# Performance work log

Measured on AMD Instinct MI355X. Metric: run time of the kernel, lower is better.

## Reference

```python
import jax, jax.numpy as jnp
import numpy as np

H = 32          # hidden_dim (forced by targetLayer = Linear(4*32, 1))
IN = 1          # input_size per step
T = 129         # seq_len
S = 4           # 4 parallel LSTM streams: [main, f1, f2, f3]


def setup_inputs() -> dict:
    key = jax.random.key(0)
    ks = jax.random.split(key, 16)
    sc = 1.0 / np.sqrt(H)
    u = lambda k, shape: jax.random.uniform(k, shape, jnp.float32, -sc, sc)
    inp = {
        "x": jax.random.normal(ks[0], (S, T, IN), jnp.float32),
        # layer 0 (input -> hidden), stacked over the 4 LSTMs; gate order i,f,g,o
        "Wih0": u(ks[1], (S, 4 * H, IN)),
        "Whh0": u(ks[2], (S, 4 * H, H)),
        "bih0": u(ks[3], (S, 4 * H)),
        "bhh0": u(ks[4], (S, 4 * H)),
        # layer 1 (hidden -> hidden)
        "Wih1": u(ks[5], (S, 4 * H, H)),
        "Whh1": u(ks[6], (S, 4 * H, H)),
        "bih1": u(ks[7], (S, 4 * H)),
        "bhh1": u(ks[8], (S, 4 * H)),
        # output heads
        "Wt": u(ks[9], (1, 4 * H)),
        "bt": u(ks[10], (1,)),
        "Wf1": u(ks[11], (1, H)),
        "bf1": u(ks[12], (1,)),
        "Wf2": u(ks[13], (1, H)),
        "bf2": u(ks[14], (1,)),
    }
    return inp


def _cell(xin, h, c, Wih, Whh, bih, bhh):
    # xin: [S, in], h/c: [S, H]; fused 4-stream LSTM cell, PyTorch gate order i,f,g,o
    g = jnp.einsum('sgi,si->sg', Wih, xin) + jnp.einsum('sgh,sh->sg', Whh, h) + bih + bhh
    i, f, gg, o = jnp.split(g, 4, axis=-1)
    c2 = jax.nn.sigmoid(f) * c + jax.nn.sigmoid(i) * jnp.tanh(gg)
    h2 = jax.nn.sigmoid(o) * jnp.tanh(c2)
    return h2, c2


def reference(x, Wih0, Whh0, bih0, bhh0, Wih1, Whh1, bih1, bhh1, Wt, bt, Wf1, bf1, Wf2, bf2):
    z = jnp.zeros((S, H), x.dtype)

    def step(carry, xt):
        h0, c0, h1, c1 = carry
        h0, c0 = _cell(xt, h0, c0, Wih0, Whh0, bih0, bhh0)
        h1, c1 = _cell(h0, h1, c1, Wih1, Whh1, bih1, bhh1)
        return (h0, c0, h1, c1), None

    xs = jnp.transpose(x, (1, 0, 2))  # [T, S, IN]
    (h0, c0, h1, c1), _ = jax.lax.scan(step, (z, z, z, z), xs)
    hlast = h1  # [S, H], last-step top-layer output; order: main, f1, f2, f3

    targetIn = hlast.reshape(1, S * H)          # torch.cat(...).view(-1, 4H)
    targetOut = targetIn @ Wt.T + bt            # [1, 1]
    f1Out = (hlast[1:2] @ Wf1.T + bf1).reshape(1, 1, 1)
    f2Out = (hlast[2:3] @ Wf2.T + bf2).reshape(1, 1, 1)
    f3Out = (hlast[3:4] @ Wf2.T + bf2).reshape(1, 1, 1)  # original bug: reuses featureLayer2
    return (targetOut, f1Out, f2Out, f3Out)
```

## Files before the change

### kernel.cpp

```cpp
#include <hip/hip_runtime.h>


#define HDIM 32
#define SEQT 129
#define NS 4

typedef float f32x2 __attribute__((ext_vector_type(2)));

__device__ __forceinline__ float fsig(float x) {
  return __builtin_amdgcn_rcpf(1.0f + __expf(-x));
}
__device__ __forceinline__ float swap_hi(float v) {
  auto r = __builtin_amdgcn_permlane32_swap(__float_as_int(v), __float_as_int(v),
                                            false, false);
  return __int_as_float(r[1]);
}

__device__ __forceinline__ float pkdot(const f32x2* __restrict__ w,
                                       const f32x2* __restrict__ h, float seed) {
  f32x2 a0 = {seed, 0.f}, a1 = {0.f, 0.f}, a2 = {0.f, 0.f}, a3 = {0.f, 0.f};
  #pragma unroll
  for (int j = 0; j < 4; ++j) {
    a0 = __builtin_elementwise_fma(w[4*j+0], h[4*j+0], a0);
    a1 = __builtin_elementwise_fma(w[4*j+1], h[4*j+1], a1);
    a2 = __builtin_elementwise_fma(w[4*j+2], h[4*j+2], a2);
    a3 = __builtin_elementwise_fma(w[4*j+3], h[4*j+3], a3);
  }
  const f32x2 r = (a0 + a1) + (a2 + a3);
  return r.x + r.y;
}

__global__ __launch_bounds__(256)
void lstm4_kernel(const float* __restrict__ x,
                  const float* __restrict__ Wih0, const float* __restrict__ Whh0,
                  const float* __restrict__ bih0, const float* __restrict__ bhh0,
                  const float* __restrict__ Wih1, const float* __restrict__ Whh1,
                  const float* __restrict__ bih1, const float* __restrict__ bhh1,
                  const float* __restrict__ Wt,  const float* __restrict__ bt,
                  const float* __restrict__ Wf1, const float* __restrict__ bf1,
                  const float* __restrict__ Wf2, const float* __restrict__ bf2,
                  float* __restrict__ out) {
  const int tid = threadIdx.x;
  const int s = tid >> 6;
  const int l = tid & 63;

  __shared__ float xs[NS * SEQT + 1];
  __shared__ __align__(16) float hb0[NS][HDIM];
  __shared__ __align__(16) float hb1[NS][HDIM];

  for (int i = tid; i < NS * SEQT; i += 256) xs[i] = x[i];
  if (tid == 0) xs[NS * SEQT] = 0.0f;
  for (int i = tid; i < NS * HDIM; i += 256) {
    (&hb0[0][0])[i] = 0.0f;
    (&hb1[0][0])[i] = 0.0f;
  }
  __syncthreads();

  const int r1 = s * 128 + l;
  const int r2 = s * 128 + l + 64;

  f32x2 wh0a[16], wh0b[16], wi1a[16], wi1b[16], wh1a[16], wh1b[16];
  #pragma unroll
  for (int j = 0; j < 16; ++j) {
    wh0a[j] = *(const f32x2*)(Whh0 + r1 * 32 + 2 * j);
    wh0b[j] = *(const f32x2*)(Whh0 + r2 * 32 + 2 * j);
    wi1a[j] = *(const f32x2*)(Wih1 + r1 * 32 + 2 * j);
    wi1b[j] = *(const f32x2*)(Wih1 + r2 * 32 + 2 * j);
    wh1a[j] = *(const f32x2*)(Whh1 + r1 * 32 + 2 * j);
    wh1b[j] = *(const f32x2*)(Whh1 + r2 * 32 + 2 * j);
  }
  const float wx0a = Wih0[r1];
  const float wx0b = Wih0[r2];
  const float b0a  = bih0[r1] + bhh0[r1];
  const float b0b  = bih0[r2] + bhh0[r2];
  const float b1a  = bih1[r1] + bhh1[r1];
  const float b1b  = bih1[r2] + bhh1[r2];

  const bool  lo   = (l < 32);
  const float m2   = lo ? 2.0f : 1.0f;
  const float add2 = lo ? -1.0f : 0.0f;

  float c0 = 0.0f, c1 = 0.0f;

  float xt0 = xs[s * SEQT];
  float v1 = fmaf(wx0a, xt0, b0a);
  float v2 = fmaf(wx0b, xt0, b0b);

  #pragma unroll 1
  for (int t = 0; t < SEQT; ++t) {
    f32x2 gv[16];
    #pragma unroll
    for (int j = 0; j < 16; ++j) gv[j] = *(const f32x2*)&hb1[s][2 * j];

    const float xtn = xs[s * SEQT + t + 1];

    const float a1  = fsig(v1);
    const float sv2 = fsig(v2 * m2);
    const float a2  = fmaf(sv2, m2, add2);
    const float p   = a1 * a2;
    const float swf = swap_hi(a1);
    const float swo = swap_hi(a2);
    c0 = fmaf(swf, c0, p);
    const float th0 = fmaf(fsig(2.0f * c0), 2.0f, -1.0f);
    const float h0new = swo * th0;

    if (lo) hb0[s][l] = h0new;

    f32x2 hv[16];
    #pragma unroll
    for (int j = 0; j < 16; ++j) hv[j] = *(const f32x2*)&hb0[s][2 * j];

    const float e1 = pkdot(wh1a, gv, b1a);
    const float e2 = pkdot(wh1b, gv, b1b);

    const float w1 = pkdot(wi1a, hv, e1);
    const float w2 = pkdot(wi1b, hv, e2);

    v1 = pkdot(wh0a, hv, fmaf(wx0a, xtn, b0a));
    v2 = pkdot(wh0b, hv, fmaf(wx0b, xtn, b0b));

    const float A1  = fsig(w1);
    const float sw2 = fsig(w2 * m2);
    const float A2  = fmaf(sw2, m2, add2);
    const float P   = A1 * A2;
    const float SWF = swap_hi(A1);
    const float SWO = swap_hi(A2);
    c1 = fmaf(SWF, c1, P);
    const float th1 = fmaf(fsig(2.0f * c1), 2.0f, -1.0f);
    const float h1new = SWO * th1;

    if (lo) hb1[s][l] = h1new;
  }

  __syncthreads();

  float acc = 0.0f;
  if (s == 0) {
    acc = fmaf(Wt[l], (&hb1[0][0])[l], Wt[l + 64] * (&hb1[0][0])[l + 64]);
  } else {
    const float* Wf = (s == 1) ? Wf1 : Wf2;
    if (l < HDIM) acc = Wf[l] * hb1[s][l];
  }
  #pragma unroll
  for (int off = 32; off > 0; off >>= 1) acc += __shfl_xor(acc, off);
  if (l == 0) {
    const float bias = (s == 0) ? bt[0] : ((s == 1) ? bf1[0] : bf2[0]);
    out[s] = acc + bias;
  }
}

extern "C" void kernel_launch(void* const* d_in, const int* in_sizes, int n_in,
                              void* d_out, int out_size, void* d_ws, size_t ws_size,
                              hipStream_t stream) {
  const float* x    = (const float*)d_in[0];
  const float* Wih0 = (const float*)d_in[1];
  const float* Whh0 = (const float*)d_in[2];
  const float* bih0 = (const float*)d_in[3];
  const float* bhh0 = (const float*)d_in[4];
  const float* Wih1 = (const float*)d_in[5];
  const float* Whh1 = (const float*)d_in[6];
  const float* bih1 = (const float*)d_in[7];
  const float* bhh1 = (const float*)d_in[8];
  const float* Wt   = (const float*)d_in[9];
  const float* bt   = (const float*)d_in[10];
  const float* Wf1  = (const float*)d_in[11];
  const float* bf1  = (const float*)d_in[12];
  const float* Wf2  = (const float*)d_in[13];
  const float* bf2  = (const float*)d_in[14];
  float* out = (float*)d_out;

  lstm4_kernel<<<1, 256, 0, stream>>>(x, Wih0, Whh0, bih0, bhh0,
                                      Wih1, Whh1, bih1, bhh1,
                                      Wt, bt, Wf1, bf1, Wf2, bf2, out);
}
```

Before: 154.1 us.

## Split LSTM layers across separate waves and pipeline them with barriers

Launches 512 threads so each stream gets two waves: one computes layer 0 and the other computes layer 1 for the same time step, overlapping the two layers instead of running them serially in one wave. Layer-0 hidden states are double-buffered in shared memory, and a block-wide __syncthreads per step hands them to the layer-1 wave. Each wave now holds fewer weight registers, and the shared-memory reads are widened to 4-float vectors. The trade-off is one block-wide barrier on every recurrent step.

```diff
diff --git a/kernel.cpp b/kernel.cpp
--- a/kernel.cpp
+++ b/kernel.cpp
@@ -6,6 +6,7 @@
 #define NS 4
 
 typedef float f32x2 __attribute__((ext_vector_type(2)));
+typedef float f32x4 __attribute__((ext_vector_type(4)));
 
 __device__ __forceinline__ float fsig(float x) {
   return __builtin_amdgcn_rcpf(1.0f + __expf(-x));
@@ -30,7 +31,7 @@
   return r.x + r.y;
 }
 
-__global__ __launch_bounds__(256)
+__global__ __launch_bounds__(512)
 void lstm4_kernel(const float* __restrict__ x,
                   const float* __restrict__ Wih0, const float* __restrict__ Whh0,
                   const float* __restrict__ bih0, const float* __restrict__ bhh0,
@@ -40,112 +41,126 @@
                   const float* __restrict__ Wf1, const float* __restrict__ bf1,
                   const float* __restrict__ Wf2, const float* __restrict__ bf2,
                   float* __restrict__ out) {
-  const int tid = threadIdx.x;
-  const int s = tid >> 6;
-  const int l = tid & 63;
+  const int tid  = threadIdx.x;
+  const int wid  = tid >> 6;
+  const int l    = tid & 63;
+  const int s    = wid >> 1;
+  const int role = wid & 1;
 
-  __shared__ float xs[NS * SEQT + 1];
-  __shared__ __align__(16) float hb0[NS][HDIM];
+  __shared__ float xs[NS * SEQT + 4];
+  __shared__ __align__(16) float hb0[2][NS][HDIM];
   __shared__ __align__(16) float hb1[NS][HDIM];
 
-  for (int i = tid; i < NS * SEQT; i += 256) xs[i] = x[i];
-  if (tid == 0) xs[NS * SEQT] = 0.0f;
-  for (int i = tid; i < NS * HDIM; i += 256) {
-    (&hb0[0][0])[i] = 0.0f;
-    (&hb1[0][0])[i] = 0.0f;
-  }
+  for (int i = tid; i < NS * SEQT + 4; i += 512) xs[i] = (i < NS * SEQT) ? x[i] : 0.0f;
   __syncthreads();
 
   const int r1 = s * 128 + l;
   const int r2 = s * 128 + l + 64;
 
-  f32x2 wh0a[16], wh0b[16], wi1a[16], wi1b[16], wh1a[16], wh1b[16];
-  #pragma unroll
-  for (int j = 0; j < 16; ++j) {
-    wh0a[j] = *(const f32x2*)(Whh0 + r1 * 32 + 2 * j);
-    wh0b[j] = *(const f32x2*)(Whh0 + r2 * 32 + 2 * j);
-    wi1a[j] = *(const f32x2*)(Wih1 + r1 * 32 + 2 * j);
-    wi1b[j] = *(const f32x2*)(Wih1 + r2 * 32 + 2 * j);
-    wh1a[j] = *(const f32x2*)(Whh1 + r1 * 32 + 2 * j);
-    wh1b[j] = *(const f32x2*)(Whh1 + r2 * 32 + 2 * j);
+  f32x2 wA[16], wB[16], wC[16], wD[16];
+  float wx0a = 0.f, wx0b = 0.f, b_a, b_b;
+  if (role == 0) {
+    #pragma unroll
+    for (int j = 0; j < 16; ++j) {
+      wA[j] = *(const f32x2*)(Whh0 + r1 * 32 + 2 * j);
+      wB[j] = *(const f32x2*)(Whh0 + r2 * 32 + 2 * j);
+    }
+    wx0a = Wih0[r1];
+    wx0b = Wih0[r2];
+    b_a  = bih0[r1] + bhh0[r1];
+    b_b  = bih0[r2] + bhh0[r2];
+  } else {
+    #pragma unroll
+    for (int j = 0; j < 16; ++j) {
+      wA[j] = *(const f32x2*)(Wih1 + r1 * 32 + 2 * j);
+      wB[j] = *(const f32x2*)(Wih1 + r2 * 32 + 2 * j);
+      wC[j] = *(const f32x2*)(Whh1 + r1 * 32 + 2 * j);
+      wD[j] = *(const f32x2*)(Whh1 + r2 * 32 + 2 * j);
+    }
+    b_a = bih1[r1] + bhh1[r1];
+    b_b = bih1[r2] + bhh1[r2];
   }
-  const float wx0a = Wih0[r1];
-  const float wx0b = Wih0[r2];
-  const float b0a  = bih0[r1] + bhh0[r1];
-  const float b0b  = bih0[r2] + bhh0[r2];
-  const float b1a  = bih1[r1] + bhh1[r1];
-  const float b1b  = bih1[r2] + bhh1[r2];
 
   const bool  lo   = (l < 32);
   const float m2   = lo ? 2.0f : 1.0f;
   const float add2 = lo ? -1.0f : 0.0f;
 
-  float c0 = 0.0f, c1 = 0.0f;
-
-  float xt0 = xs[s * SEQT];
-  float v1 = fmaf(wx0a, xt0, b0a);
-  float v2 = fmaf(wx0b, xt0, b0b);
+  float c = 0.0f;
+  float v1 = 0.f, v2 = 0.f;
+  f32x4 gv4[8];
+  #pragma unroll
+  for (int j = 0; j < 8; ++j) gv4[j] = (f32x4)0.f;
+  if (role == 0) {
+    const float x0 = xs[s * SEQT];
+    v1 = fmaf(wx0a, x0, b_a);
+    v2 = fmaf(wx0b, x0, b_b);
+  }
 
   #pragma unroll 1
   for (int t = 0; t < SEQT; ++t) {
-    f32x2 gv[16];
-    #pragma unroll
-    for (int j = 0; j < 16; ++j) gv[j] = *(const f32x2*)&hb1[s][2 * j];
+    if (role == 0) {
+      const float a1  = fsig(v1);
+      const float sv2 = fsig(v2 * m2);
+      const float a2  = fmaf(sv2, m2, add2);
+      const float p   = a1 * a2;
+      const float swf = swap_hi(a1);
+      const float swo = swap_hi(a2);
+      c = fmaf(swf, c, p);
+      const float th0 = fmaf(fsig(2.0f * c), 2.0f, -1.0f);
+      const float h0new = swo * th0;
+      if (lo) hb0[t & 1][s][l] = h0new;
+    }
+    __syncthreads();
+    if (role == 0) {
+      f32x4 hv4[8];
+      #pragma unroll
+      for (int j = 0; j < 8; ++j) hv4[j] = *(const f32x4*)&hb0[t & 1][s][4 * j];
+      const float xtn = xs[s * SEQT + t + 1];
+      const f32x2* hv = (const f32x2*)hv4;
+      v1 = pkdot(wA, hv, fmaf(wx0a, xtn, b_a));
+      v2 = pkdot(wB, hv, fmaf(wx0b, xtn, b_b));
+    } else {
+      f32x4 hv4[8];
+      #pragma unroll
+      for (int j = 0; j < 8; ++j) hv4[j] = *(const f32x4*)&hb0[t & 1][s][4 * j];
+      const f32x2* gv = (const f32x2*)gv4;
+      const float e1 = pkdot(wC, gv, b_a);
+      const float e2 = pkdot(wD, gv, b_b);
+      const f32x2* hv = (const f32x2*)hv4;
+      const float w1 = pkdot(wA, hv, e1);
+      const float w2 = pkdot(wB, hv, e2);
 
-    const float xtn = xs[s * SEQT + t + 1];
-
-    const float a1  = fsig(v1);
-    const float sv2 = fsig(v2 * m2);
-    const float a2  = fmaf(sv2, m2, add2);
-    const float p   = a1 * a2;
-    const float swf = swap_hi(a1);
-    const float swo = swap_hi(a2);
-    c0 = fmaf(swf, c0, p);
-    const float th0 = fmaf(fsig(2.0f * c0), 2.0f, -1.0f);
-    const float h0new = swo * th0;
-
-    if (lo) hb0[s][l] = h0new;
-
-    f32x2 hv[16];
-    #pragma unroll
-    for (int j = 0; j < 16; ++j) hv[j] = *(const f32x2*)&hb0[s][2 * j];
-
-    const float e1 = pkdot(wh1a, gv, b1a);
-    const float e2 = pkdot(wh1b, gv, b1b);
-
-    const float w1 = pkdot(wi1a, hv, e1);
-    const float w2 = pkdot(wi1b, hv, e2);
-
-    v1 = pkdot(wh0a, hv, fmaf(wx0a, xtn, b0a));
-    v2 = pkdot(wh0b, hv, fmaf(wx0b, xtn, b0b));
-
-    const float A1  = fsig(w1);
-    const float sw2 = fsig(w2 * m2);
-    const float A2  = fmaf(sw2, m2, add2);
-    const float P   = A1 * A2;
-    const float SWF = swap_hi(A1);
-    const float SWO = swap_hi(A2);
-    c1 = fmaf(SWF, c1, P);
-    const float th1 = fmaf(fsig(2.0f * c1), 2.0f, -1.0f);
-    const float h1new = SWO * th1;
-
-    if (lo) hb1[s][l] = h1new;
+      const float A1  = fsig(w1);
+      const float sw2 = fsig(w2 * m2);
+      const float A2  = fmaf(sw2, m2, add2);
+      const float P   = A1 * A2;
+      const float SWF = swap_hi(A1);
+      const float SWO = swap_hi(A2);
+      c = fmaf(SWF, c, P);
+      const float th1 = fmaf(fsig(2.0f * c), 2.0f, -1.0f);
+      const float h1new = SWO * th1;
+      if (lo) hb1[s][l] = h1new;
+      #pragma unroll
+      for (int j = 0; j < 8; ++j) gv4[j] = *(const f32x4*)&hb1[s][4 * j];
+    }
   }
 
   __syncthreads();
-
-  float acc = 0.0f;
-  if (s == 0) {
-    acc = fmaf(Wt[l], (&hb1[0][0])[l], Wt[l + 64] * (&hb1[0][0])[l + 64]);
-  } else {
-    const float* Wf = (s == 1) ? Wf1 : Wf2;
-    if (l < HDIM) acc = Wf[l] * hb1[s][l];
-  }
-  #pragma unroll
-  for (int off = 32; off > 0; off >>= 1) acc += __shfl_xor(acc, off);
-  if (l == 0) {
-    const float bias = (s == 0) ? bt[0] : ((s == 1) ? bf1[0] : bf2[0]);
-    out[s] = acc + bias;
+  if (tid < 256) {
+    const int hs = tid >> 6;
+    float acc = 0.0f;
+    if (hs == 0) {
+      acc = fmaf(Wt[l], (&hb1[0][0])[l], Wt[l + 64] * (&hb1[0][0])[l + 64]);
+    } else {
+      const float* Wf = (hs == 1) ? Wf1 : Wf2;
+      if (l < HDIM) acc = Wf[l] * hb1[hs][l];
+    }
+    #pragma unroll
+    for (int off = 32; off > 0; off >>= 1) acc += __shfl_xor(acc, off);
+    if (l == 0) {
+      const float bias = (hs == 0) ? bt[0] : ((hs == 1) ? bf1[0] : bf2[0]);
+      out[hs] = acc + bias;
+    }
   }
 }
 
@@ -169,7 +184,7 @@
   const float* bf2  = (const float*)d_in[14];
   float* out = (float*)d_out;
 
-  lstm4_kernel<<<1, 256, 0, stream>>>(x, Wih0, Whh0, bih0, bhh0,
+  lstm4_kernel<<<1, 512, 0, stream>>>(x, Wih0, Whh0, bih0, bhh0,
                                       Wih1, Whh1, bih1, bhh1,
                                       Wt, bt, Wf1, bf1, Wf2, bf2, out);
 }
```

Measured after the change: 160.0 us. 3.8% more time.
